# Kernel tuning notes

Hardware: AMD Instinct MI355X
Metric: run time of the kernel (lower is better)

## Reference

```python
import jax, jax.numpy as jnp
from jax import lax
import numpy as np

B, H, W, DIM = 16, 56, 56, 128
DI, K, R, N = 128, 4, 4, 1  # d_inner, directions, dt_rank, d_state


def setup_inputs() -> dict:
    key = jax.random.key(0)
    ks = jax.random.split(key, 8)
    x = jax.random.normal(ks[0], (B, H, W, DIM), dtype=jnp.float32)
    in_proj_w = jax.random.normal(ks[1], (2 * DI, DIM), dtype=jnp.float32) * 0.02
    conv_w = jax.random.normal(ks[2], (DI, 1, 3, 3), dtype=jnp.float32) * 0.1  # depthwise 3x3
    conv_b = jnp.zeros((DI,), dtype=jnp.float32)
    x_proj_w = jax.random.normal(ks[3], (K, R + 2 * N, DI), dtype=jnp.float32) * 0.02
    dt_proj_w = jax.random.normal(ks[4], (K, DI, R), dtype=jnp.float32) * 0.1
    dt_proj_b = jax.random.normal(ks[5], (K, DI), dtype=jnp.float32) * 0.1
    A_log = jnp.log(jax.random.uniform(ks[6], (K, DI, N), minval=0.5, maxval=4.0))
    Ds = jnp.ones((K, DI), dtype=jnp.float32)
    out_norm_w = jnp.ones((DI,), dtype=jnp.float32)
    out_norm_b = jnp.zeros((DI,), dtype=jnp.float32)
    return {"x": x, "in_proj_w": in_proj_w, "conv_w": conv_w, "conv_b": conv_b,
            "x_proj_w": x_proj_w, "dt_proj_w": dt_proj_w, "dt_proj_b": dt_proj_b,
            "A_log": A_log, "Ds": Ds, "out_norm_w": out_norm_w, "out_norm_b": out_norm_b}


def _ss2d(x, in_proj_w, conv_w, conv_b, x_proj_w, dt_proj_w, dt_proj_b, A_log, Ds, out_norm_w, out_norm_b):
    b, h, w, _ = x.shape
    L = h * w
    # in_proj (no bias) -> split into ssm branch and gate z
    xz = x @ in_proj_w.T                      # (B,H,W,2*DI)
    xi, z = jnp.split(xz, 2, axis=-1)
    # depthwise conv 3x3 + SiLU
    xc = jnp.transpose(xi, (0, 3, 1, 2))      # (B,DI,H,W)
    xc = lax.conv_general_dilated(xc, conv_w, (1, 1), 'SAME',
                                  feature_group_count=DI,
                                  dimension_numbers=('NCHW', 'OIHW', 'NCHW'))
    xc = jax.nn.silu(xc + conv_b[None, :, None, None])
    # 4-directional cross-scan: h, h_flip, v (transpose), v_flip
    x_hw = xc.reshape(b, DI, L)
    x_wh = jnp.transpose(xc, (0, 1, 3, 2)).reshape(b, DI, L)
    xs = jnp.stack([x_hw, jnp.flip(x_hw, -1), x_wh, jnp.flip(x_wh, -1)], axis=1)  # (B,K,DI,L)
    # per-direction input-dependent dt, B, C
    x_dbl = jnp.einsum('bkdl,kcd->bkcl', xs, x_proj_w)            # (B,K,R+2N,L)
    dt_r, Bm, Cm = jnp.split(x_dbl, [R, R + N], axis=2)
    dt = jnp.einsum('bkrl,kdr->bkdl', dt_r, dt_proj_w) + dt_proj_b[None, :, :, None]
    dt = jax.nn.softplus(dt)                                      # (B,K,DI,L)
    A = -jnp.exp(A_log)                                           # (K,DI,N)
    dA = jnp.exp(dt[..., None] * A[None, :, :, None, :])          # (B,K,DI,L,N)
    dBu = dt[..., None] * jnp.swapaxes(Bm, 2, 3)[:, :, None, :, :] * xs[..., None]
    # sequential selective scan over L (vectorized over B,K,DI,N)
    dA_l = jnp.moveaxis(dA, 3, 0)                                 # (L,B,K,DI,N)
    dBu_l = jnp.moveaxis(dBu, 3, 0)
    C_l = jnp.moveaxis(Cm, 3, 0)                                  # (L,B,K,N)

    def step(hst, inp):
        da, dbu, c = inp
        hst = da * hst + dbu
        y = jnp.sum(hst * c[:, :, None, :], axis=-1)              # (B,K,DI)
        return hst, y

    h0 = jnp.zeros((b, K, DI, N), dtype=x.dtype)
    _, ys = lax.scan(step, h0, (dA_l, dBu_l, C_l))                # ys: (L,B,K,DI)
    y = jnp.transpose(ys, (1, 2, 3, 0)) + Ds[None, :, :, None] * xs  # (B,K,DI,L)
    # merge directions back to row-major and sum
    y_h = y[:, 0]
    y_hf = jnp.flip(y[:, 1], -1)
    y_v = jnp.transpose(y[:, 2].reshape(b, DI, w, h), (0, 1, 3, 2)).reshape(b, DI, L)
    y_vf = jnp.transpose(jnp.flip(y[:, 3], -1).reshape(b, DI, w, h), (0, 1, 3, 2)).reshape(b, DI, L)
    ysum = (y_h + y_hf + y_v + y_vf).reshape(b, DI, h, w)
    ysum = jnp.transpose(ysum, (0, 2, 3, 1))                      # (B,H,W,DI)
    # out LayerNorm + gate
    mu = jnp.mean(ysum, axis=-1, keepdims=True)
    var = jnp.mean(jnp.square(ysum - mu), axis=-1, keepdims=True)
    yn = (ysum - mu) * lax.rsqrt(var + 1e-5) * out_norm_w + out_norm_b
    return yn * jax.nn.silu(z)                                    # (B,H,W,DI)


def reference(x, in_proj_w, conv_w, conv_b, x_proj_w, dt_proj_w, dt_proj_b, A_log, Ds, out_norm_w, out_norm_b):
    y = _ss2d(x, in_proj_w, conv_w, conv_b, x_proj_w, dt_proj_w, dt_proj_b, A_log, Ds, out_norm_w, out_norm_b)
    # adaptive avg pool to (1,1) then flatten -> (B, DI)
    return jnp.mean(y, axis=(1, 2))
```

## Files before the change

kernel.cpp:

```cpp
#include <hip/hip_runtime.h>
#include <math.h>

#define BB   16
#define HHH  56
#define WWW  56
#define LL   3136
#define DI_  128
#define KK   4
#define NCH  98
#define CS   32

#define OFF_XI   ((size_t)0)
#define OFF_ZS   ((size_t)6422528)
#define OFF_XC   ((size_t)12845056)
#define OFF_XDN  ((size_t)19267584)
#define OFF_PA   ((size_t)20873216)
#define OFF_HL   ((size_t)21676032)
#define OFF_H0   ((size_t)22478848)
#define OFF_CWT  ((size_t)23281664)

typedef short s16x8 __attribute__((ext_vector_type(8)));
typedef float f32x4 __attribute__((ext_vector_type(4)));

__device__ __forceinline__ float sigmoidf_(float x) { return 1.0f / (1.0f + __expf(-x)); }
__device__ __forceinline__ float softplus_(float x) {
    return fmaxf(x, 0.0f) + __logf(1.0f + __expf(-fabsf(x)));
}

__device__ __forceinline__ void bf16split(float f, short* hi, short* lo) {
    unsigned u = __float_as_uint(f);
    unsigned r = u + 0x7FFFu + ((u >> 16) & 1u);
    *hi = (short)(r >> 16);
    float hf = __uint_as_float(r & 0xFFFF0000u);
    float l  = f - hf;
    unsigned u2 = __float_as_uint(l);
    unsigned r2 = u2 + 0x7FFFu + ((u2 >> 16) & 1u);
    *lo = (short)(r2 >> 16);
}

__global__ __launch_bounds__(256) void k_wsplit(const float* __restrict__ Wp,
                                                const float* __restrict__ cw,
                                                short* __restrict__ Whi,
                                                short* __restrict__ Wlo,
                                                float* __restrict__ cwT)
{
    const int idx = blockIdx.x * 256 + threadIdx.x;
    if (idx < 256 * 128) {
        short h, l;
        bf16split(Wp[idx], &h, &l);
        Whi[idx] = h;
        Wlo[idx] = l;
    }
    if (idx < 9 * 128) {
        const int t = idx >> 7;
        const int d = idx & 127;
        cwT[t * 128 + d] = cw[d * 9 + t];
    }
}

#define APAD 136
__global__ __launch_bounds__(256) void k_inproj(const float* __restrict__ x,
                                                const short* __restrict__ Whi,
                                                const short* __restrict__ Wlo,
                                                float* __restrict__ xi,
                                                float* __restrict__ zs)
{
    __shared__ short Ahi[64 * APAD];
    __shared__ short Alo[64 * APAD];
    const int tid  = threadIdx.x;
    const int row0 = blockIdx.x * 64;

#pragma unroll
    for (int i = 0; i < 8; ++i) {
        const int idx4 = i * 256 + tid;
        const int row  = idx4 >> 5;
        const int k4   = (idx4 & 31) * 4;
        float4 v = *(const float4*)&x[(size_t)(row0 + row) * 128 + k4];
        const float f[4] = {v.x, v.y, v.z, v.w};
#pragma unroll
        for (int j = 0; j < 4; ++j) {
            short h, l;
            bf16split(f[j], &h, &l);
            Ahi[row * APAD + k4 + j] = h;
            Alo[row * APAD + k4 + j] = l;
        }
    }
    __syncthreads();

    const int w    = tid >> 6;
    const int lane = tid & 63;
    const int lr   = lane & 15;
    const int lk   = (lane >> 4) * 8;

    for (int cg = 0; cg < 4; ++cg) {
        const int col0 = cg * 64 + w * 16;
        s16x8 bhi[4], blo[4];
#pragma unroll
        for (int ks = 0; ks < 4; ++ks) {
            const size_t wo = (size_t)(col0 + lr) * 128 + ks * 32 + lk;
            bhi[ks] = *(const s16x8*)&Whi[wo];
            blo[ks] = *(const s16x8*)&Wlo[wo];
        }
#pragma unroll
        for (int rt = 0; rt < 4; ++rt) {
            f32x4 acc = {0.f, 0.f, 0.f, 0.f};
#pragma unroll
            for (int ks = 0; ks < 4; ++ks) {
                const int ao = (rt * 16 + lr) * APAD + ks * 32 + lk;
                s16x8 ahi = *(const s16x8*)&Ahi[ao];
                s16x8 alo = *(const s16x8*)&Alo[ao];
                acc = __builtin_amdgcn_mfma_f32_16x16x32_bf16(alo, bhi[ks], acc, 0, 0, 0);
                acc = __builtin_amdgcn_mfma_f32_16x16x32_bf16(ahi, blo[ks], acc, 0, 0, 0);
                acc = __builtin_amdgcn_mfma_f32_16x16x32_bf16(ahi, bhi[ks], acc, 0, 0, 0);
            }
            const int col = col0 + lr;
#pragma unroll
            for (int j = 0; j < 4; ++j) {
                const size_t row = row0 + rt * 16 + (lane >> 4) * 4 + j;
                const float v = acc[j];
                if (col < 128) {
                    xi[row * 128 + col] = v;
                } else {
                    zs[row * 128 + (col - 128)] = v * sigmoidf_(v);
                }
            }
        }
    }
}

__global__ __launch_bounds__(256) void k_conv4(const float* __restrict__ xi,
                                               const float* __restrict__ cwT,
                                               const float* __restrict__ cb,
                                               float* __restrict__ xc)
{
    const int wid = (blockIdx.x & 7) * 196 + (blockIdx.x >> 3);
    const int idx = wid * 256 + threadIdx.x;
    const int d0  = (idx & 31) * 4;
    int rest = idx >> 5;
    const int w  = rest % WWW;
    rest /= WWW;
    const int hq = rest % 14;
    const int b  = rest / 14;
    const int h0 = hq * 4;

    float4 wt[9];
#pragma unroll
    for (int t = 0; t < 9; ++t) wt[t] = *(const float4*)&cwT[t * 128 + d0];
    const float4 bias = *(const float4*)&cb[d0];

    float4 a0 = bias, a1 = bias, a2 = bias, a3 = bias;
    const float* base = &xi[(size_t)b * LL * 128 + d0];
#pragma unroll
    for (int dr = -1; dr <= 4; ++dr) {
        const int hh = h0 + dr;
        if (hh < 0 || hh >= HHH) continue;
#pragma unroll
        for (int dc = -1; dc <= 1; ++dc) {
            const int ww = w + dc;
            if (ww < 0 || ww >= WWW) continue;
            const float4 v = *(const float4*)&base[(size_t)(hh * WWW + ww) * 128];
#pragma unroll
            for (int r = 0; r < 4; ++r) {
                const int tap = dr - r;
                if (tap < -1 || tap > 1) continue;
                const float4 wv = wt[(tap + 1) * 3 + (dc + 1)];
                float4* a = (r == 0) ? &a0 : (r == 1) ? &a1 : (r == 2) ? &a2 : &a3;
                a->x = fmaf(v.x, wv.x, a->x);
                a->y = fmaf(v.y, wv.y, a->y);
                a->z = fmaf(v.z, wv.z, a->z);
                a->w = fmaf(v.w, wv.w, a->w);
            }
        }
    }
    float4 av[4] = {a0, a1, a2, a3};
#pragma unroll
    for (int r = 0; r < 4; ++r) {
        float4 o;
        o.x = av[r].x * sigmoidf_(av[r].x);
        o.y = av[r].y * sigmoidf_(av[r].y);
        o.z = av[r].z * sigmoidf_(av[r].z);
        o.w = av[r].w * sigmoidf_(av[r].w);
        *(float4*)&xc[((size_t)b * LL + (h0 + r) * WWW + w) * 128 + d0] = o;
    }
}

__global__ __launch_bounds__(256) void k_projN(const float* __restrict__ xc,
                                               const float* __restrict__ xpw,
                                               float* __restrict__ xdn)
{
    __shared__ float xs[64 * 129];
    __shared__ float wl[24 * 128];
    const int tid = threadIdx.x;
    const int b   = blockIdx.x / 49;
    const int p0  = (blockIdx.x % 49) * 64;

    for (int i = tid; i < 24 * 128; i += 256) wl[i] = xpw[i];

#pragma unroll
    for (int i = 0; i < 8; ++i) {
        const int idx4 = i * 256 + tid;
        const int row  = idx4 >> 5;
        const int d4   = (idx4 & 31) * 4;
        float4 v = *(const float4*)&xc[((size_t)b * LL + p0 + row) * 128 + d4];
        xs[row * 129 + d4 + 0] = v.x;
        xs[row * 129 + d4 + 1] = v.y;
        xs[row * 129 + d4 + 2] = v.z;
        xs[row * 129 + d4 + 3] = v.w;
    }
    __syncthreads();

    const int ks   = tid >> 6;
    const int lane = tid & 63;
    float a0 = 0.f, a1 = 0.f, a2 = 0.f, a3 = 0.f, a4 = 0.f, a5 = 0.f;
    const float* wb = &wl[ks * 6 * 128];
#pragma unroll 4
    for (int d = 0; d < 128; ++d) {
        const float xv = xs[lane * 129 + d];
        a0 = fmaf(xv, wb[0 * 128 + d], a0);
        a1 = fmaf(xv, wb[1 * 128 + d], a1);
        a2 = fmaf(xv, wb[2 * 128 + d], a2);
        a3 = fmaf(xv, wb[3 * 128 + d], a3);
        a4 = fmaf(xv, wb[4 * 128 + d], a4);
        a5 = fmaf(xv, wb[5 * 128 + d], a5);
    }
    float* o = &xdn[((size_t)(b * LL + p0 + lane)) * 32 + ks * 8];
    o[0] = a0; o[1] = a1; o[2] = a2; o[3] = a3; o[4] = a4; o[5] = a5;
}

__global__ __launch_bounds__(128) void k_scan1m(const float* __restrict__ xc,
                                                const float* __restrict__ xdn,
                                                const float* __restrict__ dtw_g,
                                                const float* __restrict__ dtb_g,
                                                const float* __restrict__ alog,
                                                float* __restrict__ Pa,
                                                float* __restrict__ Hl)
{
    __shared__ float xds[CS * 16];
    const int mode = blockIdx.x / (BB * NCH);
    const int rem  = blockIdx.x % (BB * NCH);
    const int b = rem / NCH;
    const int c = rem % NCH;
    const int d = threadIdx.x;
    const int c2 = NCH - 1 - c;
    const int l0a = c * CS;
    const int kA = mode * 2;
    const int kB = kA + 1;
    const int bkA = b * 4 + kA, bkB = b * 4 + kB;

    const float* xcb  = &xc[(size_t)b * LL * 128];
    const float* base = &xdn[(size_t)b * LL * 32];

    {
        const int row = d >> 2;
        const int q   = (d & 3) * 4;
        int prow;
        if (mode == 0) prow = l0a + row;
        else { const int l = l0a + row; prow = (l % HHH) * WWW + (l / HHH); }
        *(float4*)&xds[row * 16 + q] = *(const float4*)&base[(size_t)prow * 32 + mode * 16 + q];
    }
    __syncthreads();

    int pj[CS];
    if (mode == 0) {
#pragma unroll
        for (int i = 0; i < CS; ++i) pj[i] = l0a + i;
    } else {
#pragma unroll
        for (int i = 0; i < CS; ++i) {
            const int l = l0a + i;
            pj[i] = (l % HHH) * WWW + (l / HHH);
        }
    }
    float xv[CS];
#pragma unroll
    for (int i = 0; i < CS; ++i) xv[i] = xcb[(size_t)pj[i] * 128 + d];

    const float A0 = dtw_g[(kA * 128 + d) * 4 + 0];
    const float A1 = dtw_g[(kA * 128 + d) * 4 + 1];
    const float A2 = dtw_g[(kA * 128 + d) * 4 + 2];
    const float A3 = dtw_g[(kA * 128 + d) * 4 + 3];
    const float Ab = dtb_g[kA * 128 + d];
    const float An = -__expf(alog[kA * 128 + d]);
    const float B0 = dtw_g[(kB * 128 + d) * 4 + 0];
    const float B1 = dtw_g[(kB * 128 + d) * 4 + 1];
    const float B2 = dtw_g[(kB * 128 + d) * 4 + 2];
    const float B3 = dtw_g[(kB * 128 + d) * 4 + 3];
    const float Bb = dtb_g[kB * 128 + d];
    const float Bn = -__expf(alog[kB * 128 + d]);

    float PA = 1.0f, hA = 0.0f, PB = 1.0f, hB = 0.0f;
#pragma unroll
    for (int i = 0; i < CS; ++i) {
        const int j = CS - 1 - i;
        const float* rA = &xds[i * 16];
        const float* rB = &xds[j * 16 + 8];
        const float drawA = fmaf(rA[0], A0, fmaf(rA[1], A1, fmaf(rA[2], A2, fmaf(rA[3], A3, Ab))));
        const float drawB = fmaf(rB[0], B0, fmaf(rB[1], B1, fmaf(rB[2], B2, fmaf(rB[3], B3, Bb))));
        const float dtA = softplus_(drawA);
        const float dtB = softplus_(drawB);
        const float dAA = __expf(dtA * An);
        const float dAB = __expf(dtB * Bn);
        PA *= dAA;
        PB *= dAB;
        hA = fmaf(dAA, hA, dtA * rA[4] * xv[i]);
        hB = fmaf(dAB, hB, dtB * rB[4] * xv[j]);
    }
    Pa[((size_t)bkA * NCH + c)  * 128 + d] = PA;
    Hl[((size_t)bkA * NCH + c)  * 128 + d] = hA;
    Pa[((size_t)bkB * NCH + c2) * 128 + d] = PB;
    Hl[((size_t)bkB * NCH + c2) * 128 + d] = hB;
}

__global__ __launch_bounds__(128) void k_scan2(const float* __restrict__ Pa,
                                               const float* __restrict__ Hl,
                                               float* __restrict__ H0)
{
    const int bk = blockIdx.x;
    const int d  = threadIdx.x;
    float h = 0.0f;
#pragma unroll 7
    for (int c = 0; c < NCH; ++c) {
        const size_t o = ((size_t)bk * NCH + c) * 128 + d;
        H0[o] = h;
        h = fmaf(Pa[o], h, Hl[o]);
    }
}

__global__ __launch_bounds__(128) void k_scan3a(const float* __restrict__ xc,
                                                const float* __restrict__ xdn,
                                                const float* __restrict__ dtw_g,
                                                const float* __restrict__ dtb_g,
                                                const float* __restrict__ alog,
                                                const float* __restrict__ ds_g,
                                                const float* __restrict__ H0,
                                                float* __restrict__ ysum)
{
    __shared__ float xds[CS * 16];
    const int b = blockIdx.x / NCH;
    const int c = blockIdx.x % NCH;
    const int d = threadIdx.x;
    const int c2 = NCH - 1 - c;
    const int bk0 = b * 4 + 0, bk1 = b * 4 + 1;
    const int l0a = c * CS;

    const float* xcb  = &xc[(size_t)b * LL * 128];
    const float* base = &xdn[(size_t)b * LL * 32];
    float* yb = &ysum[(size_t)b * LL * 128];

    {
        const int row = d >> 2;
        const int q   = (d & 3) * 4;
        *(float4*)&xds[row * 16 + q] = *(const float4*)&base[(size_t)(l0a + row) * 32 + q];
    }
    __syncthreads();

    float xv[CS];
#pragma unroll
    for (int i = 0; i < CS; ++i) xv[i] = xcb[(size_t)(l0a + i) * 128 + d];

    const float A0 = dtw_g[(0 * 128 + d) * 4 + 0];
    const float A1 = dtw_g[(0 * 128 + d) * 4 + 1];
    const float A2 = dtw_g[(0 * 128 + d) * 4 + 2];
    const float A3 = dtw_g[(0 * 128 + d) * 4 + 3];
    const float Ab = dtb_g[0 * 128 + d];
    const float An = -__expf(alog[0 * 128 + d]);
    const float AD = ds_g[0 * 128 + d];
    const float B0 = dtw_g[(1 * 128 + d) * 4 + 0];
    const float B1 = dtw_g[(1 * 128 + d) * 4 + 1];
    const float B2 = dtw_g[(1 * 128 + d) * 4 + 2];
    const float B3 = dtw_g[(1 * 128 + d) * 4 + 3];
    const float Bb = dtb_g[1 * 128 + d];
    const float Bn = -__expf(alog[1 * 128 + d]);
    const float BD = ds_g[1 * 128 + d];

    float y[CS];
#pragma unroll
    for (int i = 0; i < CS; ++i) y[i] = 0.0f;

    float hA = H0[((size_t)bk0 * NCH + c)  * 128 + d];
    float hB = H0[((size_t)bk1 * NCH + c2) * 128 + d];
#pragma unroll
    for (int i = 0; i < CS; ++i) {
        const int j = CS - 1 - i;
        const float* rA = &xds[i * 16];
        const float* rB = &xds[j * 16 + 8];
        const float drawA = fmaf(rA[0], A0, fmaf(rA[1], A1, fmaf(rA[2], A2, fmaf(rA[3], A3, Ab))));
        const float drawB = fmaf(rB[0], B0, fmaf(rB[1], B1, fmaf(rB[2], B2, fmaf(rB[3], B3, Bb))));
        const float dtA = softplus_(drawA);
        const float dtB = softplus_(drawB);
        const float dAA = __expf(dtA * An);
        const float dAB = __expf(dtB * Bn);
        hA = fmaf(dAA, hA, dtA * rA[4] * xv[i]);
        hB = fmaf(dAB, hB, dtB * rB[4] * xv[j]);
        y[i] += fmaf(hA, rA[5], AD * xv[i]);
        y[j] += fmaf(hB, rB[5], BD * xv[j]);
    }
#pragma unroll
    for (int i = 0; i < CS; ++i)
        yb[(size_t)(l0a + i) * 128 + d] = y[i];
}

__global__ __launch_bounds__(128) void k_scan3b(const float* __restrict__ xc,
                                                const float* __restrict__ xdn,
                                                const float* __restrict__ dtw_g,
                                                const float* __restrict__ dtb_g,
                                                const float* __restrict__ alog,
                                                const float* __restrict__ ds_g,
                                                const float* __restrict__ H0,
                                                float* __restrict__ ysum)
{
    __shared__ float xds[CS * 16];
    const int b = blockIdx.x / NCH;
    const int c = blockIdx.x % NCH;
    const int d = threadIdx.x;
    const int c2 = NCH - 1 - c;
    const int bk2 = b * 4 + 2, bk3 = b * 4 + 3;
    const int l0a = c * CS;

    const float* xcb  = &xc[(size_t)b * LL * 128];
    const float* base = &xdn[(size_t)b * LL * 32];
    float* yb = &ysum[(size_t)b * LL * 128];

    {
        const int row = d >> 2;
        const int q   = (d & 3) * 4;
        const int l   = l0a + row;
        const int prow = (l % HHH) * WWW + (l / HHH);
        *(float4*)&xds[row * 16 + q] = *(const float4*)&base[(size_t)prow * 32 + 16 + q];
    }
    __syncthreads();

    int pj[CS];
#pragma unroll
    for (int i = 0; i < CS; ++i) {
        const int l = l0a + i;
        pj[i] = (l % HHH) * WWW + (l / HHH);
    }
    float xv[CS];
#pragma unroll
    for (int i = 0; i < CS; ++i) xv[i] = xcb[(size_t)pj[i] * 128 + d];

    const float A0 = dtw_g[(2 * 128 + d) * 4 + 0];
    const float A1 = dtw_g[(2 * 128 + d) * 4 + 1];
    const float A2 = dtw_g[(2 * 128 + d) * 4 + 2];
    const float A3 = dtw_g[(2 * 128 + d) * 4 + 3];
    const float Ab = dtb_g[2 * 128 + d];
    const float An = -__expf(alog[2 * 128 + d]);
    const float AD = ds_g[2 * 128 + d];
    const float B0 = dtw_g[(3 * 128 + d) * 4 + 0];
    const float B1 = dtw_g[(3 * 128 + d) * 4 + 1];
    const float B2 = dtw_g[(3 * 128 + d) * 4 + 2];
    const float B3 = dtw_g[(3 * 128 + d) * 4 + 3];
    const float Bb = dtb_g[3 * 128 + d];
    const float Bn = -__expf(alog[3 * 128 + d]);
    const float BD = ds_g[3 * 128 + d];

    float y[CS];
#pragma unroll
    for (int i = 0; i < CS; ++i) y[i] = 0.0f;

    float hA = H0[((size_t)bk2 * NCH + c)  * 128 + d];
    float hB = H0[((size_t)bk3 * NCH + c2) * 128 + d];
#pragma unroll
    for (int i = 0; i < CS; ++i) {
        const int j = CS - 1 - i;
        const float* rA = &xds[i * 16];
        const float* rB = &xds[j * 16 + 8];
        const float drawA = fmaf(rA[0], A0, fmaf(rA[1], A1, fmaf(rA[2], A2, fmaf(rA[3], A3, Ab))));
        const float drawB = fmaf(rB[0], B0, fmaf(rB[1], B1, fmaf(rB[2], B2, fmaf(rB[3], B3, Bb))));
        const float dtA = softplus_(drawA);
        const float dtB = softplus_(drawB);
        const float dAA = __expf(dtA * An);
        const float dAB = __expf(dtB * Bn);
        hA = fmaf(dAA, hA, dtA * rA[4] * xv[i]);
        hB = fmaf(dAB, hB, dtB * rB[4] * xv[j]);
        y[i] += fmaf(hA, rA[5], AD * xv[i]);
        y[j] += fmaf(hB, rB[5], BD * xv[j]);
    }
#pragma unroll
    for (int i = 0; i < CS; ++i)
        atomicAdd(&yb[(size_t)pj[i] * 128 + d], y[i]);
}

__global__ __launch_bounds__(256) void k_final(const float* __restrict__ ysum,
                                               const float* __restrict__ zs,
                                               const float* __restrict__ onw,
                                               const float* __restrict__ onb,
                                               float* __restrict__ out)
{
    const int wid  = threadIdx.x >> 6;
    const int lane = threadIdx.x & 63;
    const int b     = blockIdx.x / 49;
    const int chunk = blockIdx.x % 49;
    const int pbase = chunk * 64 + wid * 16;

    const float w0 = onw[lane], w1 = onw[lane + 64];
    const float b0 = onb[lane], b1 = onb[lane + 64];

    float acc0 = 0.0f, acc1 = 0.0f;
    for (int i = 0; i < 16; ++i) {
        const int p = pbase + i;
        const float v0 = ysum[((size_t)b * LL + p) * 128 + lane];
        const float v1 = ysum[((size_t)b * LL + p) * 128 + lane + 64];
        float s = v0 + v1;
#pragma unroll
        for (int off = 32; off >= 1; off >>= 1) s += __shfl_xor(s, off, 64);
        const float mu = s * (1.0f / 128.0f);
        const float d0 = v0 - mu, d1 = v1 - mu;
        float sq = d0 * d0 + d1 * d1;
#pragma unroll
        for (int off = 32; off >= 1; off >>= 1) sq += __shfl_xor(sq, off, 64);
        const float rstd = rsqrtf(sq * (1.0f / 128.0f) + 1e-5f);
        const float yn0 = fmaf(d0 * rstd, w0, b0);
        const float yn1 = fmaf(d1 * rstd, w1, b1);
        const float g0 = zs[((size_t)b * LL + p) * 128 + lane];
        const float g1 = zs[((size_t)b * LL + p) * 128 + lane + 64];
        acc0 = fmaf(yn0, g0, acc0);
        acc1 = fmaf(yn1, g1, acc1);
    }
    atomicAdd(&out[b * 128 + lane],      acc0 * (1.0f / (float)LL));
    atomicAdd(&out[b * 128 + lane + 64], acc1 * (1.0f / (float)LL));
}

extern "C" void kernel_launch(void* const* d_in, const int* in_sizes, int n_in,
                              void* d_out, int out_size, void* d_ws, size_t ws_size,
                              hipStream_t stream)
{
    const float* x     = (const float*)d_in[0];
    const float* ipw   = (const float*)d_in[1];
    const float* cw    = (const float*)d_in[2];
    const float* cb    = (const float*)d_in[3];
    const float* xpw   = (const float*)d_in[4];
    const float* dtw   = (const float*)d_in[5];
    const float* dtb   = (const float*)d_in[6];
    const float* alog  = (const float*)d_in[7];
    const float* dsg   = (const float*)d_in[8];
    const float* onw   = (const float*)d_in[9];
    const float* onb   = (const float*)d_in[10];
    float* out = (float*)d_out;

    float* ws   = (float*)d_ws;
    float* xi   = ws + OFF_XI;
    float* zs   = ws + OFF_ZS;
    float* xc   = ws + OFF_XC;
    float* xdn  = ws + OFF_XDN;
    float* Pa   = ws + OFF_PA;
    float* Hl   = ws + OFF_HL;
    float* H0   = ws + OFF_H0;
    float* cwT  = ws + OFF_CWT;
    float* ysum = xi;
    short* Whi = (short*)(ws + OFF_XC);
    short* Wlo = (short*)(ws + OFF_XC + 16384);

    hipMemsetAsync(out, 0, (size_t)out_size * 4, stream);

    k_wsplit<<<128, 256, 0, stream>>>(ipw, cw, Whi, Wlo, cwT);
    k_inproj<<<784, 256, 0, stream>>>(x, Whi, Wlo, xi, zs);

    k_conv4<<<1568, 256, 0, stream>>>(xi, cwT, cb, xc);

    k_projN<<<BB * 49, 256, 0, stream>>>(xc, xpw, xdn);

    k_scan1m<<<2 * BB * NCH, 128, 0, stream>>>(xc, xdn, dtw, dtb, alog, Pa, Hl);
    k_scan2<<<BB * KK, 128, 0, stream>>>(Pa, Hl, H0);
    k_scan3a<<<BB * NCH, 128, 0, stream>>>(xc, xdn, dtw, dtb, alog, dsg, H0, ysum);
    k_scan3b<<<BB * NCH, 128, 0, stream>>>(xc, xdn, dtw, dtb, alog, dsg, H0, ysum);

    k_final<<<BB * 49, 256, 0, stream>>>(ysum, zs, onw, onb, out);
}
```

Baseline: 257.0 us.

## Fuse vertical-direction scan with LayerNorm, gate and mean pooling

The vertical-scan kernel no longer atomically adds its results into the full ysum buffer. It reads the horizontal partial sums that scan3a already wrote at the transposed positions, adds its own contributions, and applies the LayerNorm, SiLU gate and average pooling in place. This removes the separate final kernel and one full read-modify-write pass over ysum. In exchange, each of the 32 positions per block needs two cross-wave reductions with __syncthreads, and the ysum/zs reads are strided because of the transpose. The unroll factor of the chunk-carry scan loop is also raised.

```diff
diff --git a/kernel.cpp b/kernel.cpp
--- a/kernel.cpp
+++ b/kernel.cpp
@@ -318,7 +318,7 @@
     const int bk = blockIdx.x;
     const int d  = threadIdx.x;
     float h = 0.0f;
-#pragma unroll 7
+#pragma unroll 14
     for (int c = 0; c < NCH; ++c) {
         const size_t o = ((size_t)bk * NCH + c) * 128 + d;
         H0[o] = h;
@@ -400,26 +400,34 @@
         yb[(size_t)(l0a + i) * 128 + d] = y[i];
 }
 
-__global__ __launch_bounds__(128) void k_scan3b(const float* __restrict__ xc,
-                                                const float* __restrict__ xdn,
-                                                const float* __restrict__ dtw_g,
-                                                const float* __restrict__ dtb_g,
-                                                const float* __restrict__ alog,
-                                                const float* __restrict__ ds_g,
-                                                const float* __restrict__ H0,
-                                                float* __restrict__ ysum)
+__global__ __launch_bounds__(128) void k_scan3bf(const float* __restrict__ xc,
+                                                 const float* __restrict__ xdn,
+                                                 const float* __restrict__ dtw_g,
+                                                 const float* __restrict__ dtb_g,
+                                                 const float* __restrict__ alog,
+                                                 const float* __restrict__ ds_g,
+                                                 const float* __restrict__ H0,
+                                                 const float* __restrict__ ysum,
+                                                 const float* __restrict__ zs,
+                                                 const float* __restrict__ onw,
+                                                 const float* __restrict__ onb,
+                                                 float* __restrict__ out)
 {
     __shared__ float xds[CS * 16];
+    __shared__ float redS[2];
+    __shared__ float redQ[2];
     const int b = blockIdx.x / NCH;
     const int c = blockIdx.x % NCH;
     const int d = threadIdx.x;
+    const int wv = d >> 6;
     const int c2 = NCH - 1 - c;
     const int bk2 = b * 4 + 2, bk3 = b * 4 + 3;
     const int l0a = c * CS;
 
     const float* xcb  = &xc[(size_t)b * LL * 128];
     const float* base = &xdn[(size_t)b * LL * 32];
-    float* yb = &ysum[(size_t)b * LL * 128];
+    const float* yb   = &ysum[(size_t)b * LL * 128];
+    const float* zb   = &zs[(size_t)b * LL * 128];
 
     {
         const int row = d >> 2;
@@ -477,49 +485,34 @@
         y[i] += fmaf(hA, rA[5], AD * xv[i]);
         y[j] += fmaf(hB, rB[5], BD * xv[j]);
     }
+
 #pragma unroll
     for (int i = 0; i < CS; ++i)
-        atomicAdd(&yb[(size_t)pj[i] * 128 + d], y[i]);
-}
-
-__global__ __launch_bounds__(256) void k_final(const float* __restrict__ ysum,
-                                               const float* __restrict__ zs,
-                                               const float* __restrict__ onw,
-                                               const float* __restrict__ onb,
-                                               float* __restrict__ out)
-{
-    const int wid  = threadIdx.x >> 6;
-    const int lane = threadIdx.x & 63;
-    const int b     = blockIdx.x / 49;
-    const int chunk = blockIdx.x % 49;
-    const int pbase = chunk * 64 + wid * 16;
-
-    const float w0 = onw[lane], w1 = onw[lane + 64];
-    const float b0 = onb[lane], b1 = onb[lane + 64];
-
-    float acc0 = 0.0f, acc1 = 0.0f;
-    for (int i = 0; i < 16; ++i) {
-        const int p = pbase + i;
-        const float v0 = ysum[((size_t)b * LL + p) * 128 + lane];
-        const float v1 = ysum[((size_t)b * LL + p) * 128 + lane + 64];
-        float s = v0 + v1;
+        y[i] += yb[(size_t)pj[i] * 128 + d];
+
+    const float wd = onw[d];
+    const float bd = onb[d];
+    float acc = 0.0f;
+    for (int i = 0; i < CS; ++i) {
+        const float yt = y[i];
+        float s = yt;
 #pragma unroll
         for (int off = 32; off >= 1; off >>= 1) s += __shfl_xor(s, off, 64);
-        const float mu = s * (1.0f / 128.0f);
-        const float d0 = v0 - mu, d1 = v1 - mu;
-        float sq = d0 * d0 + d1 * d1;
-#pragma unroll
-        for (int off = 32; off >= 1; off >>= 1) sq += __shfl_xor(sq, off, 64);
-        const float rstd = rsqrtf(sq * (1.0f / 128.0f) + 1e-5f);
-        const float yn0 = fmaf(d0 * rstd, w0, b0);
-        const float yn1 = fmaf(d1 * rstd, w1, b1);
-        const float g0 = zs[((size_t)b * LL + p) * 128 + lane];
-        const float g1 = zs[((size_t)b * LL + p) * 128 + lane + 64];
-        acc0 = fmaf(yn0, g0, acc0);
-        acc1 = fmaf(yn1, g1, acc1);
-    }
-    atomicAdd(&out[b * 128 + lane],      acc0 * (1.0f / (float)LL));
-    atomicAdd(&out[b * 128 + lane + 64], acc1 * (1.0f / (float)LL));
+        if ((d & 63) == 0) redS[wv] = s;
+        __syncthreads();
+        const float mu = (redS[0] + redS[1]) * (1.0f / 128.0f);
+        const float dv = yt - mu;
+        float q = dv * dv;
+#pragma unroll
+        for (int off = 32; off >= 1; off >>= 1) q += __shfl_xor(q, off, 64);
+        if ((d & 63) == 0) redQ[wv] = q;
+        __syncthreads();
+        const float var  = (redQ[0] + redQ[1]) * (1.0f / 128.0f);
+        const float rstd = rsqrtf(var + 1e-5f);
+        const float yn   = fmaf(dv * rstd, wd, bd);
+        acc = fmaf(yn, zb[(size_t)pj[i] * 128 + d], acc);
+    }
+    atomicAdd(&out[b * 128 + d], acc * (1.0f / (float)LL));
 }
 
 extern "C" void kernel_launch(void* const* d_in, const int* in_sizes, int n_in,
@@ -564,7 +557,6 @@
     k_scan1m<<<2 * BB * NCH, 128, 0, stream>>>(xc, xdn, dtw, dtb, alog, Pa, Hl);
     k_scan2<<<BB * KK, 128, 0, stream>>>(Pa, Hl, H0);
     k_scan3a<<<BB * NCH, 128, 0, stream>>>(xc, xdn, dtw, dtb, alog, dsg, H0, ysum);
-    k_scan3b<<<BB * NCH, 128, 0, stream>>>(xc, xdn, dtw, dtb, alog, dsg, H0, ysum);
-
-    k_final<<<BB * 49, 256, 0, stream>>>(ysum, zs, onw, onb, out);
-}
+    k_scan3bf<<<BB * NCH, 128, 0, stream>>>(xc, xdn, dtw, dtb, alog, dsg, H0, ysum,
+                                            zs, onw, onb, out);
+}
```

Measured after the change: 322.8 us. 25.6% more time.
